# Kernel tuning notes

Measured on AMD Instinct MI355X. Metric: run time of the kernel, lower is better.

The kernel has to match this reference:

```python
import jax, jax.numpy as jnp
import numpy as np

N_HEADS = 16
HEAD = 64
SEQ = 2048
EMBED = 1024
BATCH = 4

def setup_inputs() -> dict:
    key = jax.random.key(0)
    ks = jax.random.split(key, 6)
    inputs = jax.random.normal(ks[0], (BATCH, SEQ, EMBED), dtype=jnp.float32)
    # per-head projection weights stacked: [H, E, D] (nn.Linear(E, D, bias=False))
    s = 1.0 / np.sqrt(EMBED)
    Wq = jax.random.uniform(ks[1], (N_HEADS, EMBED, HEAD), jnp.float32, -s, s)
    Wk = jax.random.uniform(ks[2], (N_HEADS, EMBED, HEAD), jnp.float32, -s, s)
    Wv = jax.random.uniform(ks[3], (N_HEADS, EMBED, HEAD), jnp.float32, -s, s)
    Wo = jax.random.uniform(ks[4], (EMBED, EMBED), jnp.float32, -s, s)
    bo = jax.random.uniform(ks[5], (EMBED,), jnp.float32, -s, s)
    return {"inputs": inputs, "Wq": Wq, "Wk": Wk, "Wv": Wv, "Wo": Wo, "bo": bo}

def reference(inputs, Wq, Wk, Wv, Wo, bo):
    B, S, E = inputs.shape
    # batched per-head projections: [B,S,E] x [H,E,D] -> [B,H,S,D]
    q = jnp.einsum('bse,hed->bhsd', inputs, Wq)
    k = jnp.einsum('bse,hed->bhsd', inputs, Wk)
    v = jnp.einsum('bse,hed->bhsd', inputs, Wv)
    q = q / jnp.sqrt(jnp.float32(HEAD)).astype(q.dtype)
    scores = jnp.einsum('bhsd,bhtd->bhst', q, k)  # [B,H,S,S]
    causal = jnp.tril(jnp.ones((S, S), dtype=bool))
    scores = jnp.where(causal, scores, jnp.finfo(scores.dtype).min)
    weights = jax.nn.softmax(scores, axis=-1)
    out = jnp.einsum('bhst,bhtd->bhsd', weights, v)  # [B,H,S,D]
    # concat heads in head order -> [B,S,H*D]
    out = jnp.transpose(out, (0, 2, 1, 3)).reshape(B, S, N_HEADS * HEAD)
    return out @ Wo.T + bo
```

## Files before the change

kernel.cpp:

```cpp
#include <hip/hip_runtime.h>
#include <stdint.h>

typedef unsigned short ushort_t;
typedef __attribute__((ext_vector_type(8))) short short8;
typedef __attribute__((ext_vector_type(4))) short bf16x4;
typedef __attribute__((ext_vector_type(4))) float f32x4;
typedef __attribute__((ext_vector_type(16))) float f32x16;

#define AS1 __attribute__((address_space(1)))
#define AS3 __attribute__((address_space(3)))

__device__ __forceinline__ void gl_lds16(const void* g, void* l) {
    __builtin_amdgcn_global_load_lds((const AS1 unsigned int*)g,
                                     (AS3 unsigned int*)l, 16, 0, 0);
}

__device__ __forceinline__ ushort_t f2bf(float f) {
    union { float f; unsigned u; } v; v.f = f;
    unsigned r = v.u + 0x7fffu + ((v.u >> 16) & 1u);
    return (ushort_t)(r >> 16);
}

__device__ __forceinline__ unsigned cvt_pk_bf16(float lo, float hi) {
    unsigned r;
    asm("v_cvt_pk_bf16_f32 %0, %1, %2" : "=v"(r) : "v"(lo), "v"(hi));
    return r;
}

__global__ __launch_bounds__(256) void prep_k(const float* __restrict__ inp,
                                              const float* __restrict__ Wo,
                                              const float* __restrict__ Wq,
                                              const float* __restrict__ Wk,
                                              const float* __restrict__ Wv,
                                              ushort_t* __restrict__ inp_bf,
                                              ushort_t* __restrict__ WoB,
                                              ushort_t* __restrict__ WT) {
    const int bx = blockIdx.x, tid = threadIdx.x;
    if (bx < 4608) {
        const float* src = (bx < 4096) ? inp : Wo;
        ushort_t* dst    = (bx < 4096) ? inp_bf : WoB;
        int i = ((bx < 4096 ? bx : bx - 4096) * 256 + tid) * 8;
        float4 a = *(const float4*)(src + i);
        float4 b = *(const float4*)(src + i + 4);
        short8 o;
        o[0] = (short)f2bf(a.x); o[1] = (short)f2bf(a.y);
        o[2] = (short)f2bf(a.z); o[3] = (short)f2bf(a.w);
        o[4] = (short)f2bf(b.x); o[5] = (short)f2bf(b.y);
        o[6] = (short)f2bf(b.z); o[7] = (short)f2bf(b.w);
        *(short8*)(dst + i) = o;
        return;
    }
    __shared__ ushort_t t[64 * 65];
    const int wb = bx - 4608;
    const int mat = wb >> 8;
    const int h   = (wb >> 4) & 15;
    const int et  = wb & 15;
    const float* W = (mat == 0 ? Wq : (mat == 1 ? Wk : Wv)) + h * (1024 * 64);
    const float* src = W + et * 64 * 64;
#pragma unroll
    for (int i = 0; i < 16; ++i) {
        int idx = i * 256 + tid;
        int e = idx >> 6, d = idx & 63;
        t[e * 65 + d] = f2bf(src[idx]);
    }
    __syncthreads();
    ushort_t* dst = WT + (mat * 16 + h) * (64 * 1024) + et * 64;
#pragma unroll
    for (int i = 0; i < 16; ++i) {
        int idx = i * 256 + tid;
        int d = idx >> 6, e = idx & 63;
        dst[d * 1024 + e] = t[e * 65 + d];
    }
}

__global__ __launch_bounds__(512, 4) void qkv_k(const ushort_t* __restrict__ A,
                                                const ushort_t* __restrict__ WT,
                                                ushort_t* __restrict__ Q,
                                                ushort_t* __restrict__ K,
                                                ushort_t* __restrict__ Vt) {
    __shared__ __align__(16) ushort_t ring[36864];
    const int tid = threadIdx.x, wave = tid >> 6, lane = tid & 63;
    const int ln15 = lane & 15, quad = lane >> 4;
    const int wm = wave >> 1, wn = wave & 1;
    const int m0 = blockIdx.x * 256, n0 = blockIdx.y * 128;

    const int sa_row  = wave * 16 + (lane >> 2);
    const int sa_colS = (((lane & 3) ^ ((lane >> 3) & 3))) * 8;
    const int woff    = wave * 512;
    const int rchunk  = (quad ^ ((ln15 >> 1) & 3)) * 8;

    f32x4 acc[4][4];
#pragma unroll
    for (int i = 0; i < 4; ++i)
#pragma unroll
        for (int j = 0; j < 4; ++j)
#pragma unroll
            for (int e = 0; e < 4; ++e) acc[i][j][e] = 0.f;

    auto stage = [&](int t, ushort_t* buf) {
        const int kb = t * 32;
        gl_lds16(A  + (size_t)(m0 + sa_row)       * 1024 + kb + sa_colS, buf + woff);
        gl_lds16(A  + (size_t)(m0 + 128 + sa_row) * 1024 + kb + sa_colS, buf + 4096 + woff);
        gl_lds16(WT + (size_t)(n0 + sa_row)       * 1024 + kb + sa_colS, buf + 8192 + woff);
    };

    stage(0, &ring[0]); stage(1, &ring[12288]);
    asm volatile("s_waitcnt vmcnt(3)" ::: "memory");
    __builtin_amdgcn_s_barrier();
    __builtin_amdgcn_sched_barrier(0);

    auto phase = [&](int t, const ushort_t* bufC, ushort_t* bufS) {
        short8 a[4], b[4];
#pragma unroll
        for (int f = 0; f < 4; ++f)
            a[f] = *(const short8*)&bufC[(wm * 64 + f * 16 + ln15) * 32 + rchunk];
#pragma unroll
        for (int f = 0; f < 4; ++f)
            b[f] = *(const short8*)&bufC[8192 + (wn * 64 + f * 16 + ln15) * 32 + rchunk];
        if (t + 2 < 32) stage(t + 2, bufS);
        if (t < 30)       asm volatile("s_waitcnt vmcnt(3)" ::: "memory");
        else if (t == 30) asm volatile("s_waitcnt vmcnt(0)" ::: "memory");
        __builtin_amdgcn_sched_barrier(0);
        __builtin_amdgcn_s_setprio(1);
#pragma unroll
        for (int fm = 0; fm < 4; ++fm)
#pragma unroll
            for (int fn = 0; fn < 4; ++fn)
                acc[fm][fn] = __builtin_amdgcn_mfma_f32_16x16x32_bf16(a[fm], b[fn], acc[fm][fn], 0, 0, 0);
        __builtin_amdgcn_s_setprio(0);
        __builtin_amdgcn_s_barrier();
        __builtin_amdgcn_sched_barrier(0);
    };

    for (int t3 = 0; t3 < 30; t3 += 3) {
        phase(t3,     &ring[0],     &ring[24576]);
        phase(t3 + 1, &ring[12288], &ring[0]);
        phase(t3 + 2, &ring[24576], &ring[12288]);
    }
    phase(30, &ring[0],     &ring[24576]);
    phase(31, &ring[12288], &ring[0]);

    const int n_base = n0 + wn * 64;
    const int mat = n_base >> 10;
    const int h   = (n_base >> 6) & 15;
    if (mat < 2) {
        ushort_t* dst = (mat == 0) ? Q : K;
        const float scale = (mat == 0) ? 0.125f : 1.0f;
#pragma unroll
        for (int fm = 0; fm < 4; ++fm) {
#pragma unroll
            for (int r = 0; r < 4; ++r) {
                int mg = m0 + wm * 64 + fm * 16 + quad * 4 + r;
                int bi = mg >> 11, s = mg & 2047;
                size_t base = ((size_t)(bi * 16 + h) * 2048 + s) * 64;
#pragma unroll
                for (int fn = 0; fn < 4; ++fn)
                    dst[base + fn * 16 + ln15] = f2bf(acc[fm][fn][r] * scale);
            }
        }
    } else {
        ushort_t* tb = &ring[wave * 4608];
#pragma unroll
        for (int fn = 0; fn < 4; ++fn)
#pragma unroll
            for (int fm = 0; fm < 4; ++fm) {
                uint2 w;
                w.x = cvt_pk_bf16(acc[fm][fn][0], acc[fm][fn][1]);
                w.y = cvt_pk_bf16(acc[fm][fn][2], acc[fm][fn][3]);
                *(uint2*)&tb[(fn * 16 + ln15) * 72 + fm * 16 + quad * 4] = w;
            }
        const int s0 = m0 + wm * 64;
        const int bi = s0 >> 11, sb = s0 & 2047;
#pragma unroll
        for (int p = 0; p < 8; ++p) {
            int d  = p * 8 + (lane >> 3);
            int sc = (lane & 7) * 8;
            short8 vv = *(const short8*)&tb[d * 72 + sc];
            *(short8*)&Vt[((size_t)(bi * 16 + h) * 64 + d) * 2048 + sb + sc] = vv;
        }
    }
}

__global__ __launch_bounds__(256, 3) void flash_k(const ushort_t* Q, const ushort_t* K,
                                                  const ushort_t* Vt, ushort_t* Aout) {
    __shared__ __align__(16) ushort_t KVs[3][2][64 * 64];
    const int tid = threadIdx.x, wave = tid >> 6, lane = tid & 63;
    const int ln31 = lane & 31, h = lane >> 5;
    const int bx = blockIdx.x;
    const int qt = 15 - (bx >> 6);
    const int bh = bx & 63;
    const int qw = qt * 128 + wave * 32;
    const ushort_t* Kb = K + (size_t)bh * 2048 * 64;
    const ushort_t* Vb = Vt + (size_t)bh * 64 * 2048;
    const int srow = tid >> 3, c8 = (tid & 7) * 8;
    const int c8s  = ((tid & 7) ^ ((tid >> 3) & 7)) * 8;
    const int swr  = ln31 & 7;

    short8 qf[4];
    {
        const ushort_t* Qb = Q + (size_t)bh * 2048 * 64;
#pragma unroll
        for (int c = 0; c < 4; ++c)
            qf[c] = *(const short8*)&Qb[(size_t)(qw + ln31) * 64 + c * 16 + h * 8];
    }

    f32x16 o[2];
#pragma unroll
    for (int dt = 0; dt < 2; ++dt)
#pragma unroll
        for (int e = 0; e < 16; ++e) o[dt][e] = 0.f;
    float l_s = 0.f;

    auto stageKV = [&](int kn, int slot) {
        gl_lds16(Kb + (size_t)(kn * 64 + srow) * 64 + c8s,        &KVs[slot][0][srow * 64 + c8]);
        gl_lds16(Kb + (size_t)(kn * 64 + 32 + srow) * 64 + c8s,   &KVs[slot][0][(32 + srow) * 64 + c8]);
        gl_lds16(Vb + (size_t)srow * 2048 + kn * 64 + c8s,        &KVs[slot][1][srow * 64 + c8]);
        gl_lds16(Vb + (size_t)(32 + srow) * 2048 + kn * 64 + c8s, &KVs[slot][1][(32 + srow) * 64 + c8]);
    };

    const int ktEnd = 2 * qt + 2;
    stageKV(0, 0); stageKV(1, 1);
    asm volatile("s_waitcnt vmcnt(4)" ::: "memory");
    __builtin_amdgcn_s_barrier();
    __builtin_amdgcn_sched_barrier(0);

    int cur = 0;
    for (int kt = 0; kt < ktEnd; ++kt) {
        int s2 = cur + 2; if (s2 >= 3) s2 -= 3;
        if (kt + 2 < ktEnd) stageKV(kt + 2, s2);
        if (kt * 64 <= qw + 31) {
            const ushort_t* Ksc = KVs[cur][0];
            const ushort_t* Vsc = KVs[cur][1];
            unsigned W[2][8];
            const bool diag = (kt * 64 + 63 > qw);
            const int qg = qw + ln31;
#pragma unroll
            for (int kt2 = 0; kt2 < 2; ++kt2) {
                f32x16 sc;
#pragma unroll
                for (int e = 0; e < 16; ++e) sc[e] = 0.f;
                __builtin_amdgcn_s_setprio(1);
#pragma unroll
                for (int c = 0; c < 4; ++c) {
                    short8 kf = *(const short8*)&Ksc[(kt2 * 32 + ln31) * 64 + ((2 * c + h) ^ swr) * 8];
                    sc = __builtin_amdgcn_mfma_f32_32x32x16_bf16(kf, qf[c], sc, 0, 0, 0);
                }
                __builtin_amdgcn_s_setprio(0);
                if (diag) {
#pragma unroll
                    for (int r = 0; r < 16; ++r) {
                        int kg = kt * 64 + kt2 * 32 + (r & 3) + 8 * (r >> 2) + 4 * h;
                        if (kg > qg) sc[r] = -1e30f;
                    }
                }
#pragma unroll
                for (int g = 0; g < 4; ++g) {
                    float p0 = __expf(sc[4 * g + 0]);
                    float p1 = __expf(sc[4 * g + 1]);
                    float p2 = __expf(sc[4 * g + 2]);
                    float p3 = __expf(sc[4 * g + 3]);
                    l_s += (p0 + p1) + (p2 + p3);
                    W[kt2][2 * g]     = cvt_pk_bf16(p0, p1);
                    W[kt2][2 * g + 1] = cvt_pk_bf16(p2, p3);
                }
            }
            short8 pb[4];
#pragma unroll
            for (int t = 0; t < 2; ++t)
#pragma unroll
                for (int x = 0; x < 2; ++x) {
                    unsigned a0 = W[t][4 * x + 0], b0 = W[t][4 * x + 2];
                    unsigned a1 = W[t][4 * x + 1], b1 = W[t][4 * x + 3];
                    asm volatile("v_permlane32_swap_b32 %0, %1" : "+v"(a0), "+v"(b0));
                    asm volatile("v_permlane32_swap_b32 %0, %1" : "+v"(a1), "+v"(b1));
                    union { unsigned u[4]; short8 s; } u;
                    u.u[0] = a0; u.u[1] = a1; u.u[2] = b0; u.u[3] = b1;
                    pb[t * 2 + x] = u.s;
                }
            __builtin_amdgcn_s_setprio(1);
#pragma unroll
            for (int dt = 0; dt < 2; ++dt)
#pragma unroll
                for (int x = 0; x < 4; ++x) {
                    short8 vf = *(const short8*)&Vsc[(dt * 32 + ln31) * 64 + ((2 * x + h) ^ swr) * 8];
                    o[dt] = __builtin_amdgcn_mfma_f32_32x32x16_bf16(vf, pb[x], o[dt], 0, 0, 0);
                }
            __builtin_amdgcn_s_setprio(0);
        }
        if (kt < ktEnd - 2)       asm volatile("s_waitcnt vmcnt(4)" ::: "memory");
        else if (kt == ktEnd - 2) asm volatile("s_waitcnt vmcnt(0)" ::: "memory");
        __builtin_amdgcn_s_barrier();
        __builtin_amdgcn_sched_barrier(0);
        cur = (cur + 1 == 3) ? 0 : cur + 1;
    }
    l_s += __shfl_xor(l_s, 32);
    float inv = 1.f / l_s;
    ushort_t* myO = &KVs[0][0][0] + wave * 2304;
#pragma unroll
    for (int dt = 0; dt < 2; ++dt)
#pragma unroll
        for (int g = 0; g < 4; ++g) {
            unsigned w0 = cvt_pk_bf16(o[dt][4 * g + 0] * inv, o[dt][4 * g + 1] * inv);
            unsigned w1 = cvt_pk_bf16(o[dt][4 * g + 2] * inv, o[dt][4 * g + 3] * inv);
            int d0 = 8 * g + 4 * h + 32 * dt;
            *(unsigned*)&myO[ln31 * 72 + d0]     = w0;
            *(unsigned*)&myO[ln31 * 72 + d0 + 2] = w1;
        }
    const int bi = bh >> 4, hh = bh & 15;
#pragma unroll
    for (int p = 0; p < 4; ++p) {
        int row = p * 8 + (lane >> 3);
        int cc = (lane & 7) * 8;
        short8 vv = *(const short8*)&myO[row * 72 + cc];
        int qg2 = qw + row;
        *(short8*)&Aout[((size_t)bi * 2048 + qg2) * 1024 + hh * 64 + cc] = vv;
    }
}

__global__ __launch_bounds__(512, 6) void outproj_k(const ushort_t* __restrict__ A,
                                                    const ushort_t* __restrict__ WoB,
                                                    const float* __restrict__ bo,
                                                    float* __restrict__ Out) {
    __shared__ __align__(16) ushort_t ring[24576];
    const int tid = threadIdx.x, wave = tid >> 6, lane = tid & 63;
    const int ln15 = lane & 15, quad = lane >> 4;
    const int wm = wave >> 1, wn = wave & 1;
    const int m0 = blockIdx.x * 128, n0 = blockIdx.y * 128;

    const int sa_row  = wave * 16 + (lane >> 2);
    const int sa_colS = (((lane & 3) ^ ((lane >> 3) & 3))) * 8;
    const int woff    = wave * 512;
    const int rchunk  = (quad ^ ((ln15 >> 1) & 3)) * 8;

    f32x4 acc[2][4];
#pragma unroll
    for (int i = 0; i < 2; ++i)
#pragma unroll
        for (int j = 0; j < 4; ++j)
#pragma unroll
            for (int e = 0; e < 4; ++e) acc[i][j][e] = 0.f;

    auto stage = [&](int t, ushort_t* buf) {
        const int kb = t * 32;
        gl_lds16(A   + (size_t)(m0 + sa_row) * 1024 + kb + sa_colS, buf + woff);
        gl_lds16(WoB + (size_t)(n0 + sa_row) * 1024 + kb + sa_colS, buf + 4096 + woff);
    };

    stage(0, &ring[0]); stage(1, &ring[8192]);
    asm volatile("s_waitcnt vmcnt(2)" ::: "memory");
    __builtin_amdgcn_s_barrier();
    __builtin_amdgcn_sched_barrier(0);

    auto phase = [&](int t, const ushort_t* bufC, ushort_t* bufS) {
        short8 a[2], b[4];
#pragma unroll
        for (int f = 0; f < 2; ++f)
            a[f] = *(const short8*)&bufC[(wm * 32 + f * 16 + ln15) * 32 + rchunk];
#pragma unroll
        for (int f = 0; f < 4; ++f)
            b[f] = *(const short8*)&bufC[4096 + (wn * 64 + f * 16 + ln15) * 32 + rchunk];
        if (t + 2 < 32) stage(t + 2, bufS);
        if (t < 30)       asm volatile("s_waitcnt vmcnt(2)" ::: "memory");
        else if (t == 30) asm volatile("s_waitcnt vmcnt(0)" ::: "memory");
        __builtin_amdgcn_sched_barrier(0);
        __builtin_amdgcn_s_setprio(1);
#pragma unroll
        for (int fm = 0; fm < 2; ++fm)
#pragma unroll
            for (int fn = 0; fn < 4; ++fn)
                acc[fm][fn] = __builtin_amdgcn_mfma_f32_16x16x32_bf16(a[fm], b[fn], acc[fm][fn], 0, 0, 0);
        __builtin_amdgcn_s_setprio(0);
        __builtin_amdgcn_s_barrier();
        __builtin_amdgcn_sched_barrier(0);
    };

    for (int t3 = 0; t3 < 30; t3 += 3) {
        phase(t3,     &ring[0],     &ring[16384]);
        phase(t3 + 1, &ring[8192],  &ring[0]);
        phase(t3 + 2, &ring[16384], &ring[8192]);
    }
    phase(30, &ring[0],    &ring[16384]);
    phase(31, &ring[8192], &ring[0]);

    const int nb = n0 + wn * 64;
    float bias[4];
#pragma unroll
    for (int fn = 0; fn < 4; ++fn) bias[fn] = bo[nb + fn * 16 + ln15];
#pragma unroll
    for (int fm = 0; fm < 2; ++fm)
#pragma unroll
        for (int r = 0; r < 4; ++r) {
            int mg = m0 + wm * 32 + fm * 16 + quad * 4 + r;
#pragma unroll
            for (int fn = 0; fn < 4; ++fn)
                Out[(size_t)mg * 1024 + nb + fn * 16 + ln15] = acc[fm][fn][r] + bias[fn];
        }
}

extern "C" void kernel_launch(void* const* d_in, const int* in_sizes, int n_in,
                              void* d_out, int out_size, void* d_ws, size_t ws_size,
                              hipStream_t stream) {
    (void)in_sizes; (void)n_in; (void)out_size; (void)ws_size;
    const float* inp = (const float*)d_in[0];
    const float* Wq  = (const float*)d_in[1];
    const float* Wk  = (const float*)d_in[2];
    const float* Wv  = (const float*)d_in[3];
    const float* Wo  = (const float*)d_in[4];
    const float* bo  = (const float*)d_in[5];
    float* out = (float*)d_out;

    ushort_t* ws = (ushort_t*)d_ws;
    ushort_t* R0  = ws;
    ushort_t* WT  = R0  + 8388608;
    ushort_t* WoB = WT  + 3145728;
    ushort_t* Qb  = WoB + 1048576;
    ushort_t* Kb  = Qb  + 8388608;
    ushort_t* Vtb = Kb  + 8388608;

    ushort_t* inp_bf = R0;
    ushort_t* At     = R0;

    prep_k<<<5376, 256, 0, stream>>>(inp, Wo, Wq, Wk, Wv, inp_bf, WoB, WT);
    qkv_k<<<dim3(32, 24), 512, 0, stream>>>(inp_bf, WT, Qb, Kb, Vtb);
    flash_k<<<dim3(1024), 256, 0, stream>>>(Qb, Kb, Vtb, At);
    outproj_k<<<dim3(64, 8), 512, 0, stream>>>(At, WoB, bo, out);
}
```

Baseline: 214.6 us.

## Shrink QKV GEMM tile and flash KV ring to raise occupancy

Result: slower. 227.8 us (+6.2%).

```diff
diff --git a/kernel.cpp b/kernel.cpp
--- a/kernel.cpp
+++ b/kernel.cpp
@@ -73,25 +73,25 @@
     }
 }
 
-__global__ __launch_bounds__(512, 4) void qkv_k(const ushort_t* __restrict__ A,
+__global__ __launch_bounds__(512, 6) void qkv_k(const ushort_t* __restrict__ A,
                                                 const ushort_t* __restrict__ WT,
                                                 ushort_t* __restrict__ Q,
                                                 ushort_t* __restrict__ K,
                                                 ushort_t* __restrict__ Vt) {
-    __shared__ __align__(16) ushort_t ring[36864];
+    __shared__ __align__(16) ushort_t ring[24576];
     const int tid = threadIdx.x, wave = tid >> 6, lane = tid & 63;
     const int ln15 = lane & 15, quad = lane >> 4;
     const int wm = wave >> 1, wn = wave & 1;
-    const int m0 = blockIdx.x * 256, n0 = blockIdx.y * 128;
+    const int m0 = blockIdx.x * 128, n0 = blockIdx.y * 128;
 
     const int sa_row  = wave * 16 + (lane >> 2);
     const int sa_colS = (((lane & 3) ^ ((lane >> 3) & 3))) * 8;
     const int woff    = wave * 512;
     const int rchunk  = (quad ^ ((ln15 >> 1) & 3)) * 8;
 
-    f32x4 acc[4][4];
-#pragma unroll
-    for (int i = 0; i < 4; ++i)
+    f32x4 acc[2][4];
+#pragma unroll
+    for (int i = 0; i < 2; ++i)
 #pragma unroll
         for (int j = 0; j < 4; ++j)
 #pragma unroll
@@ -99,31 +99,30 @@
 
     auto stage = [&](int t, ushort_t* buf) {
         const int kb = t * 32;
-        gl_lds16(A  + (size_t)(m0 + sa_row)       * 1024 + kb + sa_colS, buf + woff);
-        gl_lds16(A  + (size_t)(m0 + 128 + sa_row) * 1024 + kb + sa_colS, buf + 4096 + woff);
-        gl_lds16(WT + (size_t)(n0 + sa_row)       * 1024 + kb + sa_colS, buf + 8192 + woff);
+        gl_lds16(A  + (size_t)(m0 + sa_row) * 1024 + kb + sa_colS, buf + woff);
+        gl_lds16(WT + (size_t)(n0 + sa_row) * 1024 + kb + sa_colS, buf + 4096 + woff);
     };
 
-    stage(0, &ring[0]); stage(1, &ring[12288]);
-    asm volatile("s_waitcnt vmcnt(3)" ::: "memory");
+    stage(0, &ring[0]); stage(1, &ring[8192]);
+    asm volatile("s_waitcnt vmcnt(2)" ::: "memory");
     __builtin_amdgcn_s_barrier();
     __builtin_amdgcn_sched_barrier(0);
 
     auto phase = [&](int t, const ushort_t* bufC, ushort_t* bufS) {
-        short8 a[4], b[4];
+        short8 a[2], b[4];
+#pragma unroll
+        for (int f = 0; f < 2; ++f)
+            a[f] = *(const short8*)&bufC[(wm * 32 + f * 16 + ln15) * 32 + rchunk];
 #pragma unroll
         for (int f = 0; f < 4; ++f)
-            a[f] = *(const short8*)&bufC[(wm * 64 + f * 16 + ln15) * 32 + rchunk];
-#pragma unroll
-        for (int f = 0; f < 4; ++f)
-            b[f] = *(const short8*)&bufC[8192 + (wn * 64 + f * 16 + ln15) * 32 + rchunk];
+            b[f] = *(const short8*)&bufC[4096 + (wn * 64 + f * 16 + ln15) * 32 + rchunk];
         if (t + 2 < 32) stage(t + 2, bufS);
-        if (t < 30)       asm volatile("s_waitcnt vmcnt(3)" ::: "memory");
+        if (t < 30)       asm volatile("s_waitcnt vmcnt(2)" ::: "memory");
         else if (t == 30) asm volatile("s_waitcnt vmcnt(0)" ::: "memory");
         __builtin_amdgcn_sched_barrier(0);
         __builtin_amdgcn_s_setprio(1);
 #pragma unroll
-        for (int fm = 0; fm < 4; ++fm)
+        for (int fm = 0; fm < 2; ++fm)
 #pragma unroll
             for (int fn = 0; fn < 4; ++fn)
                 acc[fm][fn] = __builtin_amdgcn_mfma_f32_16x16x32_bf16(a[fm], b[fn], acc[fm][fn], 0, 0, 0);
@@ -133,12 +132,12 @@
     };
 
     for (int t3 = 0; t3 < 30; t3 += 3) {
-        phase(t3,     &ring[0],     &ring[24576]);
-        phase(t3 + 1, &ring[12288], &ring[0]);
-        phase(t3 + 2, &ring[24576], &ring[12288]);
-    }
-    phase(30, &ring[0],     &ring[24576]);
-    phase(31, &ring[12288], &ring[0]);
+        phase(t3,     &ring[0],     &ring[16384]);
+        phase(t3 + 1, &ring[8192],  &ring[0]);
+        phase(t3 + 2, &ring[16384], &ring[8192]);
+    }
+    phase(30, &ring[0],    &ring[16384]);
+    phase(31, &ring[8192], &ring[0]);
 
     const int n_base = n0 + wn * 64;
     const int mat = n_base >> 10;
@@ -147,10 +146,10 @@
         ushort_t* dst = (mat == 0) ? Q : K;
         const float scale = (mat == 0) ? 0.125f : 1.0f;
 #pragma unroll
-        for (int fm = 0; fm < 4; ++fm) {
+        for (int fm = 0; fm < 2; ++fm) {
 #pragma unroll
             for (int r = 0; r < 4; ++r) {
-                int mg = m0 + wm * 64 + fm * 16 + quad * 4 + r;
+                int mg = m0 + wm * 32 + fm * 16 + quad * 4 + r;
                 int bi = mg >> 11, s = mg & 2047;
                 size_t base = ((size_t)(bi * 16 + h) * 2048 + s) * 64;
 #pragma unroll
@@ -159,31 +158,31 @@
             }
         }
     } else {
-        ushort_t* tb = &ring[wave * 4608];
+        ushort_t* tb = &ring[wave * 2560];
 #pragma unroll
         for (int fn = 0; fn < 4; ++fn)
 #pragma unroll
-            for (int fm = 0; fm < 4; ++fm) {
+            for (int fm = 0; fm < 2; ++fm) {
                 uint2 w;
                 w.x = cvt_pk_bf16(acc[fm][fn][0], acc[fm][fn][1]);
                 w.y = cvt_pk_bf16(acc[fm][fn][2], acc[fm][fn][3]);
-                *(uint2*)&tb[(fn * 16 + ln15) * 72 + fm * 16 + quad * 4] = w;
+                *(uint2*)&tb[(fn * 16 + ln15) * 40 + fm * 16 + quad * 4] = w;
             }
-        const int s0 = m0 + wm * 64;
+        const int s0 = m0 + wm * 32;
         const int bi = s0 >> 11, sb = s0 & 2047;
 #pragma unroll
-        for (int p = 0; p < 8; ++p) {
-            int d  = p * 8 + (lane >> 3);
-            int sc = (lane & 7) * 8;
-            short8 vv = *(const short8*)&tb[d * 72 + sc];
+        for (int p = 0; p < 4; ++p) {
+            int d  = p * 16 + (lane >> 2);
+            int sc = (lane & 3) * 8;
+            short8 vv = *(const short8*)&tb[d * 40 + sc];
             *(short8*)&Vt[((size_t)(bi * 16 + h) * 64 + d) * 2048 + sb + sc] = vv;
         }
     }
 }
 
-__global__ __launch_bounds__(256, 3) void flash_k(const ushort_t* Q, const ushort_t* K,
+__global__ __launch_bounds__(256, 4) void flash_k(const ushort_t* Q, const ushort_t* K,
                                                   const ushort_t* Vt, ushort_t* Aout) {
-    __shared__ __align__(16) ushort_t KVs[3][2][64 * 64];
+    __shared__ __align__(16) ushort_t KVs[2][2][64 * 64];
     const int tid = threadIdx.x, wave = tid >> 6, lane = tid & 63;
     const int ln31 = lane & 31, h = lane >> 5;
     const int bx = blockIdx.x;
@@ -211,23 +210,22 @@
         for (int e = 0; e < 16; ++e) o[dt][e] = 0.f;
     float l_s = 0.f;
 
-    auto stageKV = [&](int kn, int slot) {
-        gl_lds16(Kb + (size_t)(kn * 64 + srow) * 64 + c8s,        &KVs[slot][0][srow * 64 + c8]);
-        gl_lds16(Kb + (size_t)(kn * 64 + 32 + srow) * 64 + c8s,   &KVs[slot][0][(32 + srow) * 64 + c8]);
-        gl_lds16(Vb + (size_t)srow * 2048 + kn * 64 + c8s,        &KVs[slot][1][srow * 64 + c8]);
-        gl_lds16(Vb + (size_t)(32 + srow) * 2048 + kn * 64 + c8s, &KVs[slot][1][(32 + srow) * 64 + c8]);
-    };
-
     const int ktEnd = 2 * qt + 2;
-    stageKV(0, 0); stageKV(1, 1);
-    asm volatile("s_waitcnt vmcnt(4)" ::: "memory");
-    __builtin_amdgcn_s_barrier();
-    __builtin_amdgcn_sched_barrier(0);
-
-    int cur = 0;
+    gl_lds16(Kb + (size_t)srow * 64 + c8s,          &KVs[0][0][srow * 64 + c8]);
+    gl_lds16(Kb + (size_t)(32 + srow) * 64 + c8s,   &KVs[0][0][(32 + srow) * 64 + c8]);
+    gl_lds16(Vb + (size_t)srow * 2048 + c8s,        &KVs[0][1][srow * 64 + c8]);
+    gl_lds16(Vb + (size_t)(32 + srow) * 2048 + c8s, &KVs[0][1][(32 + srow) * 64 + c8]);
+    __syncthreads();
+
     for (int kt = 0; kt < ktEnd; ++kt) {
-        int s2 = cur + 2; if (s2 >= 3) s2 -= 3;
-        if (kt + 2 < ktEnd) stageKV(kt + 2, s2);
+        const int cur = kt & 1, nxt = cur ^ 1;
+        if (kt + 1 < ktEnd) {
+            int kn = kt + 1;
+            gl_lds16(Kb + (size_t)(kn * 64 + srow) * 64 + c8s,        &KVs[nxt][0][srow * 64 + c8]);
+            gl_lds16(Kb + (size_t)(kn * 64 + 32 + srow) * 64 + c8s,   &KVs[nxt][0][(32 + srow) * 64 + c8]);
+            gl_lds16(Vb + (size_t)srow * 2048 + kn * 64 + c8s,        &KVs[nxt][1][srow * 64 + c8]);
+            gl_lds16(Vb + (size_t)(32 + srow) * 2048 + kn * 64 + c8s, &KVs[nxt][1][(32 + srow) * 64 + c8]);
+        }
         if (kt * 64 <= qw + 31) {
             const ushort_t* Ksc = KVs[cur][0];
             const ushort_t* Vsc = KVs[cur][1];
@@ -287,11 +285,7 @@
                 }
             __builtin_amdgcn_s_setprio(0);
         }
-        if (kt < ktEnd - 2)       asm volatile("s_waitcnt vmcnt(4)" ::: "memory");
-        else if (kt == ktEnd - 2) asm volatile("s_waitcnt vmcnt(0)" ::: "memory");
-        __builtin_amdgcn_s_barrier();
-        __builtin_amdgcn_sched_barrier(0);
-        cur = (cur + 1 == 3) ? 0 : cur + 1;
+        __syncthreads();
     }
     l_s += __shfl_xor(l_s, 32);
     float inv = 1.f / l_s;
@@ -421,7 +415,7 @@
     ushort_t* At     = R0;
 
     prep_k<<<5376, 256, 0, stream>>>(inp, Wo, Wq, Wk, Wv, inp_bf, WoB, WT);
-    qkv_k<<<dim3(32, 24), 512, 0, stream>>>(inp_bf, WT, Qb, Kb, Vtb);
+    qkv_k<<<dim3(64, 24), 512, 0, stream>>>(inp_bf, WT, Qb, Kb, Vtb);
     flash_k<<<dim3(1024), 256, 0, stream>>>(Qb, Kb, Vtb, At);
     outproj_k<<<dim3(64, 8), 512, 0, stream>>>(At, WoB, bo, out);
 }
```

## Switch flash kernel K/V staging to double buffering with four blocks per CU

Applied to the files above, without the earlier changes.

New measurement: 222.5 us. 1.04x slower.

```diff
diff --git a/kernel.cpp b/kernel.cpp
--- a/kernel.cpp
+++ b/kernel.cpp
@@ -181,9 +181,9 @@
     }
 }
 
-__global__ __launch_bounds__(256, 3) void flash_k(const ushort_t* Q, const ushort_t* K,
+__global__ __launch_bounds__(256, 4) void flash_k(const ushort_t* Q, const ushort_t* K,
                                                   const ushort_t* Vt, ushort_t* Aout) {
-    __shared__ __align__(16) ushort_t KVs[3][2][64 * 64];
+    __shared__ __align__(16) ushort_t KVs[2][2][64 * 64];
     const int tid = threadIdx.x, wave = tid >> 6, lane = tid & 63;
     const int ln31 = lane & 31, h = lane >> 5;
     const int bx = blockIdx.x;
@@ -211,23 +211,22 @@
         for (int e = 0; e < 16; ++e) o[dt][e] = 0.f;
     float l_s = 0.f;
 
-    auto stageKV = [&](int kn, int slot) {
-        gl_lds16(Kb + (size_t)(kn * 64 + srow) * 64 + c8s,        &KVs[slot][0][srow * 64 + c8]);
-        gl_lds16(Kb + (size_t)(kn * 64 + 32 + srow) * 64 + c8s,   &KVs[slot][0][(32 + srow) * 64 + c8]);
-        gl_lds16(Vb + (size_t)srow * 2048 + kn * 64 + c8s,        &KVs[slot][1][srow * 64 + c8]);
-        gl_lds16(Vb + (size_t)(32 + srow) * 2048 + kn * 64 + c8s, &KVs[slot][1][(32 + srow) * 64 + c8]);
-    };
-
     const int ktEnd = 2 * qt + 2;
-    stageKV(0, 0); stageKV(1, 1);
-    asm volatile("s_waitcnt vmcnt(4)" ::: "memory");
-    __builtin_amdgcn_s_barrier();
-    __builtin_amdgcn_sched_barrier(0);
-
-    int cur = 0;
+    gl_lds16(Kb + (size_t)srow * 64 + c8s,          &KVs[0][0][srow * 64 + c8]);
+    gl_lds16(Kb + (size_t)(32 + srow) * 64 + c8s,   &KVs[0][0][(32 + srow) * 64 + c8]);
+    gl_lds16(Vb + (size_t)srow * 2048 + c8s,        &KVs[0][1][srow * 64 + c8]);
+    gl_lds16(Vb + (size_t)(32 + srow) * 2048 + c8s, &KVs[0][1][(32 + srow) * 64 + c8]);
+    __syncthreads();
+
     for (int kt = 0; kt < ktEnd; ++kt) {
-        int s2 = cur + 2; if (s2 >= 3) s2 -= 3;
-        if (kt + 2 < ktEnd) stageKV(kt + 2, s2);
+        const int cur = kt & 1, nxt = cur ^ 1;
+        if (kt + 1 < ktEnd) {
+            int kn = kt + 1;
+            gl_lds16(Kb + (size_t)(kn * 64 + srow) * 64 + c8s,        &KVs[nxt][0][srow * 64 + c8]);
+            gl_lds16(Kb + (size_t)(kn * 64 + 32 + srow) * 64 + c8s,   &KVs[nxt][0][(32 + srow) * 64 + c8]);
+            gl_lds16(Vb + (size_t)srow * 2048 + kn * 64 + c8s,        &KVs[nxt][1][srow * 64 + c8]);
+            gl_lds16(Vb + (size_t)(32 + srow) * 2048 + kn * 64 + c8s, &KVs[nxt][1][(32 + srow) * 64 + c8]);
+        }
         if (kt * 64 <= qw + 31) {
             const ushort_t* Ksc = KVs[cur][0];
             const ushort_t* Vsc = KVs[cur][1];
@@ -287,11 +286,7 @@
                 }
             __builtin_amdgcn_s_setprio(0);
         }
-        if (kt < ktEnd - 2)       asm volatile("s_waitcnt vmcnt(4)" ::: "memory");
-        else if (kt == ktEnd - 2) asm volatile("s_waitcnt vmcnt(0)" ::: "memory");
-        __builtin_amdgcn_s_barrier();
-        __builtin_amdgcn_sched_barrier(0);
-        cur = (cur + 1 == 3) ? 0 : cur + 1;
+        __syncthreads();
     }
     l_s += __shfl_xor(l_s, 32);
     float inv = 1.f / l_s;
```
